# Optimization experiments

Hardware: AMD Instinct MI355X
Metric: run time of the kernel (lower is better)

Reference implementation:

```python
import jax, jax.numpy as jnp
import numpy as np

B, L, H, D = 1, 2048, 24, 128
BLKQ = BLKK = 64
TOPK_RATIO = 0.5


def setup_inputs() -> dict:
    key = jax.random.key(0)
    kq, kk, kv, kw = jax.random.split(key, 4)
    q = jax.random.normal(kq, (B, L, H, D), jnp.float32)
    k = jax.random.normal(kk, (B, L, H, D), jnp.float32)
    v = jax.random.normal(kv, (B, L, H, D), jnp.float32)
    proj_w = jax.random.normal(kw, (D, D), jnp.float32) * 0.02  # nn.Linear weight (out,in)
    proj_b = jnp.zeros((D,), jnp.float32)
    return {"query": q, "key": k, "value": v, "proj_w": proj_w, "proj_b": proj_b}


def _block_sparse_attention(q, k, v, scale):
    # q,k,v: (B,H,L,D). Block-mean pooled QK scores pick top-k key blocks per query block.
    Nq, Nk = L // BLKQ, L // BLKK
    topk = max(1, int(Nk * TOPK_RATIO))  # real_topk
    qb = q.reshape(B, H, Nq, BLKQ, D).mean(axis=3)          # (B,H,Nq,D)
    kb = k.reshape(B, H, Nk, BLKK, D).mean(axis=3)          # (B,H,Nk,D)
    blk_scores = jnp.einsum('bhqd,bhkd->bhqk', qb, kb)      # pooled block map
    _, lut = jax.lax.top_k(blk_scores, topk)                # (B,H,Nq,topk) selected key blocks
    kblk = k.reshape(B, H, Nk, BLKK, D)
    vblk = v.reshape(B, H, Nk, BLKK, D)
    idx = lut.reshape(B, H, Nq * topk, 1, 1)
    kg = jnp.take_along_axis(kblk, idx, axis=2).reshape(B, H, Nq, topk * BLKK, D)
    vg = jnp.take_along_axis(vblk, idx, axis=2).reshape(B, H, Nq, topk * BLKK, D)
    qr = q.reshape(B, H, Nq, BLKQ, D)
    scores = jnp.einsum('bhqid,bhqjd->bhqij', qr, kg) * scale  # (B,H,Nq,BLKQ,topk*BLKK)
    attn = jax.nn.softmax(scores, axis=-1)
    o = jnp.einsum('bhqij,bhqjd->bhqid', attn, vg)
    return o.reshape(B, H, L, D)


def _linear_attention(q, k, v):
    # feature_map='softmax' over the head dim
    ql = jax.nn.softmax(q, axis=-1)
    kl = jax.nn.softmax(k, axis=-1)
    kvsum = jnp.einsum('bhld,bhle->bhde', kl, v)            # K^T V  (B,H,D,D)
    ksum = kl.sum(axis=2)                                    # (B,H,D)
    num = jnp.einsum('bhld,bhde->bhle', ql, kvsum)
    den = 1e-5 + jnp.einsum('bhld,bhd->bhl', ql, ksum)[..., None]
    return num / den


def reference(query, key, value, proj_w, proj_b):
    q = jnp.swapaxes(query, 1, 2)  # (B,H,L,D)
    k = jnp.swapaxes(key, 1, 2)
    v = jnp.swapaxes(value, 1, 2)
    scale = D ** -0.5  # softmax_scale = head_size**-0.5
    o_s = _block_sparse_attention(q, k, v, scale)
    o_l = _linear_attention(q, k, v)
    o_l = o_l @ proj_w.T + proj_b  # learnable fusion projection
    out = jnp.swapaxes(o_s + o_l, 1, 2)  # back to (B,L,H,D)
    return out
```

## Files before the change

kernel.cpp:

```cpp
#include <hip/hip_runtime.h>
#include <math.h>

#define HH 24
#define LLEN 2048
#define DD 128
#define BLK 64
#define NBLK 32
#define TOPK 16
#define NCHUNK 16

typedef __attribute__((ext_vector_type(8))) short bf16x8;
typedef __attribute__((ext_vector_type(4))) float f32x4;

typedef unsigned int u32_g __attribute__((address_space(1)));
typedef unsigned int u32_l __attribute__((address_space(3)));

__device__ __forceinline__ unsigned short f2bf(float f) {
    unsigned u = __builtin_bit_cast(unsigned, f);
    unsigned r = (u + 0x7FFFu + ((u >> 16) & 1u)) >> 16;
    return (unsigned short)r;
}
__device__ __forceinline__ float bf2f(unsigned short b) {
    unsigned u = ((unsigned)b) << 16;
    return __builtin_bit_cast(float, u);
}
__device__ __forceinline__ void gload16(unsigned short* lds, const unsigned short* g) {
    __builtin_amdgcn_global_load_lds((const u32_g*)g, (u32_l*)lds, 16, 0, 0);
}

__global__ __launch_bounds__(256) void convert_pool(
    const float* __restrict__ q, const float* __restrict__ k, const float* __restrict__ v,
    unsigned short* __restrict__ kb16, unsigned short* __restrict__ vt16,
    float* __restrict__ qb, float* __restrict__ kb)
{
    const int nb = blockIdx.x, h = blockIdx.y;
    const int l0 = nb * BLK;
    const int tid = threadIdx.x;
    __shared__ unsigned short vt_s[DD * BLK];

    {
        const int r = tid >> 2, c0 = (tid & 3) * 4;
        const float* kp = k + ((size_t)(l0 + r) * HH + h) * DD + c0 * 8;
        unsigned short* krow = kb16 + ((size_t)h * LLEN + l0 + r) * DD;
        #pragma unroll
        for (int j = 0; j < 4; ++j) {
            float4 a = *(const float4*)(kp + j * 8);
            float4 c = *(const float4*)(kp + j * 8 + 4);
            unsigned short tmp[8] = {f2bf(a.x), f2bf(a.y), f2bf(a.z), f2bf(a.w),
                                     f2bf(c.x), f2bf(c.y), f2bf(c.z), f2bf(c.w)};
            const int chunk = (c0 + j) ^ (r & 7);
            *(bf16x8*)&krow[chunk * 8] = *(bf16x8*)tmp;
        }
    }
    {
        const int kp2 = tid >> 3, dgb = tid & 7;
        const float* v0p = v + ((size_t)(l0 + kp2 * 2) * HH + h) * DD;
        const float* v1p = v0p + (size_t)HH * DD;
        #pragma unroll
        for (int j2 = 0; j2 < 4; ++j2) {
            const int d0 = dgb * 4 + j2 * 32;
            float4 a = *(const float4*)(v0p + d0);
            float4 c = *(const float4*)(v1p + d0);
            float a4[4] = {a.x, a.y, a.z, a.w}, c4[4] = {c.x, c.y, c.z, c.w};
            #pragma unroll
            for (int i = 0; i < 4; ++i) {
                unsigned pak = (unsigned)f2bf(a4[i]) | ((unsigned)f2bf(c4[i]) << 16);
                const int d = d0 + i;
                const int chunk = (kp2 >> 2) ^ (d & 7);
                *(unsigned*)&vt_s[d * BLK + chunk * 8 + (kp2 & 3) * 2] = pak;
            }
        }
    }
    __syncthreads();
    {
        bf16x8* dstv = (bf16x8*)(vt16 + (size_t)(h * NBLK + nb) * DD * BLK);
        const bf16x8* srcv = (const bf16x8*)vt_s;
        #pragma unroll
        for (int j = 0; j < 4; ++j) dstv[tid * 4 + j] = srcv[tid * 4 + j];
    }
    __syncthreads();
    {
        float* ps = (float*)vt_s;
        const int d = tid & 127, half = tid >> 7;
        const size_t rs = (size_t)HH * DD;
        const float* qp = q + ((size_t)(l0 + half * 32) * HH + h) * DD + d;
        const float* kp = k + ((size_t)(l0 + half * 32) * HH + h) * DD + d;
        float sq = 0.f, sk = 0.f;
        #pragma unroll 8
        for (int i = 0; i < 32; ++i) { sq += qp[i * rs]; sk += kp[i * rs]; }
        ps[half * 128 + d] = sq;
        ps[256 + half * 128 + d] = sk;
        __syncthreads();
        if (half == 0) {
            qb[((size_t)h * NBLK + nb) * DD + d] = ps[d] + ps[128 + d];
            kb[((size_t)h * NBLK + nb) * DD + d] = ps[256 + d] + ps[384 + d];
        }
    }
}

__global__ __launch_bounds__(256) void topk_kernel(
    const float* __restrict__ qb, const float* __restrict__ kb, int* __restrict__ lut)
{
    const int h = blockIdx.x;
    __shared__ float kb_s[NBLK][DD];
    __shared__ float sc[NBLK][NBLK];
    const int tid = threadIdx.x;
    for (int f = tid; f < NBLK * DD / 4; f += 256)
        ((float4*)kb_s)[f] = ((const float4*)(kb + (size_t)h * NBLK * DD))[f];
    __syncthreads();
    for (int p = tid; p < NBLK * NBLK; p += 256) {
        const int iq = p >> 5, ik = p & 31;
        const float4* qr4 = (const float4*)(qb + ((size_t)h * NBLK + iq) * DD);
        const float4* kr4 = (const float4*)&kb_s[ik][0];
        float s = 0.f;
        for (int dq = 0; dq < DD / 4; ++dq) {
            float4 a = qr4[dq], b = kr4[dq];
            s += a.x * b.x + a.y * b.y + a.z * b.z + a.w * b.w;
        }
        sc[iq][ik] = s;
    }
    __syncthreads();
    if (tid < NBLK) {
        const int iq = tid;
        for (int t = 0; t < TOPK; ++t) {
            float bv = -1e30f; int bi = 0;
            for (int j = 0; j < NBLK; ++j) {
                float s = sc[iq][j];
                if (s > bv) { bv = s; bi = j; }
            }
            lut[((size_t)h * NBLK + iq) * TOPK + t] = bi;
            sc[iq][bi] = -1e30f;
        }
    }
}

__global__ __launch_bounds__(256, 2) void kv_mfma(
    const float* __restrict__ k, const unsigned short* __restrict__ vt16,
    float* __restrict__ kvp, float* __restrict__ ksp)
{
    const int h = blockIdx.x, c = blockIdx.y;
    __shared__ unsigned short klT[DD * DD];
    const int tid = threadIdx.x;
    const int quad = tid >> 3, dpart = tid & 7;
    const int d0 = dpart * 16;
    const int wid = tid >> 6, lane = tid & 63;
    const int l15 = lane & 15, g = lane >> 4;

    f32x4 acc[2][8];
    #pragma unroll
    for (int mi = 0; mi < 2; ++mi)
        #pragma unroll
        for (int nt = 0; nt < 8; ++nt) acc[mi][nt] = (f32x4){0.f, 0.f, 0.f, 0.f};
    float ksa[16];
    #pragma unroll
    for (int j = 0; j < 16; ++j) ksa[j] = 0.f;

    const int l0 = c * DD;
    {
        const int lr = quad * 4;
        float rows[4][16];
        #pragma unroll
        for (int i = 0; i < 4; ++i) {
            const float4* kp4 = (const float4*)(k + ((size_t)(l0 + lr + i) * HH + h) * DD + d0);
            #pragma unroll
            for (int t4 = 0; t4 < 4; ++t4) {
                float4 x = kp4[t4];
                rows[i][t4 * 4 + 0] = x.x; rows[i][t4 * 4 + 1] = x.y;
                rows[i][t4 * 4 + 2] = x.z; rows[i][t4 * 4 + 3] = x.w;
            }
        }
        #pragma unroll
        for (int i = 0; i < 4; ++i) {
            float mx = -1e30f;
            #pragma unroll
            for (int j = 0; j < 16; ++j) mx = fmaxf(mx, rows[i][j]);
            mx = fmaxf(mx, __shfl_xor(mx, 1));
            mx = fmaxf(mx, __shfl_xor(mx, 2));
            mx = fmaxf(mx, __shfl_xor(mx, 4));
            float s = 0.f;
            #pragma unroll
            for (int j = 0; j < 16; ++j) { rows[i][j] = __expf(rows[i][j] - mx); s += rows[i][j]; }
            s += __shfl_xor(s, 1);
            s += __shfl_xor(s, 2);
            s += __shfl_xor(s, 4);
            const float rinv = 1.0f / s;
            #pragma unroll
            for (int j = 0; j < 16; ++j) { rows[i][j] *= rinv; ksa[j] += rows[i][j]; }
        }
        #pragma unroll
        for (int j = 0; j < 16; ++j) {
            const int d = d0 + j;
            unsigned long long pk =
                (unsigned long long)f2bf(rows[0][j]) |
                ((unsigned long long)f2bf(rows[1][j]) << 16) |
                ((unsigned long long)f2bf(rows[2][j]) << 32) |
                ((unsigned long long)f2bf(rows[3][j]) << 48);
            const int chunk = (quad >> 1) ^ (d & 7);
            *(unsigned long long*)&klT[d * DD + chunk * 8 + (quad & 1) * 4] = pk;
        }
    }
    __syncthreads();
    const int bkt = c * 2;
    #pragma unroll
    for (int ks = 0; ks < 4; ++ks) {
        bf16x8 af[2];
        #pragma unroll
        for (int mi = 0; mi < 2; ++mi) {
            const int d = (wid * 2 + mi) * 16 + l15;
            const int chunk = (ks * 4 + g) ^ (d & 7);
            af[mi] = *(const bf16x8*)&klT[d * DD + chunk * 8];
        }
        const int s = ks * 4 + g;
        const int kt = bkt + (s >> 3);
        #pragma unroll
        for (int nt = 0; nt < 8; ++nt) {
            const int e = nt * 16 + l15;
            const int cc = (s & 7) ^ (e & 7);
            bf16x8 bf = *(const bf16x8*)&vt16[((size_t)(h * NBLK + kt) * DD + e) * BLK + cc * 8];
            acc[0][nt] = __builtin_amdgcn_mfma_f32_16x16x32_bf16(af[0], bf, acc[0][nt], 0, 0, 0);
            acc[1][nt] = __builtin_amdgcn_mfma_f32_16x16x32_bf16(af[1], bf, acc[1][nt], 0, 0, 0);
        }
    }
    float* op = kvp + ((size_t)h * NCHUNK + c) * DD * DD;
    #pragma unroll
    for (int mi = 0; mi < 2; ++mi)
        #pragma unroll
        for (int nt = 0; nt < 8; ++nt)
            #pragma unroll
            for (int r = 0; r < 4; ++r)
                op[(size_t)((wid * 2 + mi) * 16 + g * 4 + r) * DD + nt * 16 + l15] = acc[mi][nt][r];
    #pragma unroll
    for (int j = 0; j < 16; ++j) {
        ksa[j] += __shfl_xor(ksa[j], 8);
        ksa[j] += __shfl_xor(ksa[j], 16);
        ksa[j] += __shfl_xor(ksa[j], 32);
    }
    if ((lane >> 3) == 0) {
        float* kp2 = ksp + (((size_t)h * NCHUNK + c) * 4 + wid) * DD + d0;
        #pragma unroll
        for (int j = 0; j < 16; ++j) kp2[j] = ksa[j];
    }
}

__global__ __launch_bounds__(256) void reduce_M(
    const float* __restrict__ kvp, const float* __restrict__ ksp,
    const float* __restrict__ W, unsigned short* __restrict__ Mt,
    float* __restrict__ ksumf)
{
    const int h = blockIdx.x, rb = blockIdx.y;
    __shared__ float kv_s[32][DD];
    const int tid = threadIdx.x;
    for (int f4 = tid; f4 < 32 * DD / 4; f4 += 256) {
        float4 s = make_float4(0.f, 0.f, 0.f, 0.f);
        #pragma unroll
        for (int cc = 0; cc < NCHUNK; ++cc) {
            float4 x = ((const float4*)(kvp + ((size_t)h * NCHUNK + cc) * DD * DD
                                        + (size_t)rb * 32 * DD))[f4];
            s.x += x.x; s.y += x.y; s.z += x.z; s.w += x.w;
        }
        ((float4*)kv_s)[f4] = s;
    }
    if (rb == 0 && tid < DD) {
        float s = 0.f;
        #pragma unroll
        for (int p = 0; p < NCHUNK * 4; ++p)
            s += ksp[((size_t)h * NCHUNK * 4 + p) * DD + tid];
        ksumf[(size_t)h * DD + tid] = s;
    }
    __syncthreads();
    const int e = tid & 127, dh = tid >> 7;
    float accm[16];
    #pragma unroll
    for (int i = 0; i < 16; ++i) accm[i] = 0.f;
    const float4* wr4 = (const float4*)(W + (size_t)e * DD);
    for (int c4 = 0; c4 < DD / 4; ++c4) {
        const float4 wv = wr4[c4];
        #pragma unroll
        for (int i = 0; i < 16; ++i) {
            const float4 kv4 = ((const float4*)&kv_s[dh * 16 + i][0])[c4];
            accm[i] += kv4.x * wv.x + kv4.y * wv.y + kv4.z * wv.z + kv4.w * wv.w;
        }
    }
    unsigned short* mp = Mt + (size_t)h * DD * DD + (size_t)e * DD + rb * 32 + dh * 16;
    #pragma unroll
    for (int ii = 0; ii < 16; ii += 2) {
        unsigned pk = (unsigned)f2bf(accm[ii]) | ((unsigned)f2bf(accm[ii + 1]) << 16);
        *(unsigned*)&mp[ii] = pk;
    }
}

__global__ __launch_bounds__(256, 3) void sla_attn(
    const float* __restrict__ q, const unsigned short* __restrict__ kb16,
    const unsigned short* __restrict__ vt16, const int* __restrict__ lut,
    const unsigned short* __restrict__ Mt, const float* __restrict__ ksumf,
    const float* __restrict__ pb, float* __restrict__ out)
{
    const int b = blockIdx.x;
    const int slot = b >> 3;
    const int h = (b & 7) + 8 * (slot >> 5);
    const int nq = slot & 31;

    __shared__ unsigned short Ks[BLK * DD];
    __shared__ unsigned short Vt[DD * BLK];
    __shared__ unsigned short Ps[4 * 16 * BLK];

    const int tid = threadIdx.x;
    const int wid = tid >> 6, lane = tid & 63;
    const int l15 = lane & 15, g = lane >> 4;
    const int q0 = wid * 16;

    bf16x8 qf[4];
    {
        const float scale = 0.08838834764831845f;
        const int qrow = nq * BLK + q0 + l15;
        const float* qp = q + ((size_t)qrow * HH + h) * DD;
        #pragma unroll
        for (int ks = 0; ks < 4; ++ks) {
            const int d0 = ks * 32 + g * 8;
            float4 a = *(const float4*)(qp + d0);
            float4 c = *(const float4*)(qp + d0 + 4);
            float vv[8] = {a.x, a.y, a.z, a.w, c.x, c.y, c.z, c.w};
            #pragma unroll
            for (int j = 0; j < 8; ++j)
                qf[ks][j] = (short)f2bf(vv[j] * scale);
        }
    }

    f32x4 Oacc[8];
    #pragma unroll
    for (int nt = 0; nt < 8; ++nt) Oacc[nt] = (f32x4){0.f, 0.f, 0.f, 0.f};
    float m_run = -1e30f, l_run = 0.f;

    const int* lrow = lut + ((size_t)h * NBLK + nq) * TOPK;

    {
        const int kb0 = lrow[0];
        const unsigned short* kg = kb16 + ((size_t)h * LLEN + (size_t)kb0 * BLK) * DD;
        #pragma unroll
        for (int i = 0; i < 4; ++i) {
            const int is = wid * 4 + i;
            gload16(&Ks[is * 512], kg + is * 512 + lane * 8);
        }
    }

    for (int it = 0; it < TOPK; ++it) {
        const int kbI = lrow[it];
        __builtin_amdgcn_s_barrier();
        {
            const unsigned short* vg = vt16 + (size_t)(h * NBLK + kbI) * DD * BLK;
            #pragma unroll
            for (int i = 0; i < 4; ++i) {
                const int is = wid * 4 + i;
                gload16(&Vt[is * 512], vg + is * 512 + lane * 8);
            }
        }
        asm volatile("s_waitcnt vmcnt(4)" ::: "memory");
        __builtin_amdgcn_sched_barrier(0);

        f32x4 sacc[4];
        #pragma unroll
        for (int mt = 0; mt < 4; ++mt) sacc[mt] = (f32x4){0.f, 0.f, 0.f, 0.f};
        __builtin_amdgcn_s_setprio(1);
        #pragma unroll
        for (int ks = 0; ks < 4; ++ks) {
            #pragma unroll
            for (int mt = 0; mt < 4; ++mt) {
                const int row = mt * 16 + l15;
                const int chunk = (ks * 4 + g) ^ (row & 7);
                bf16x8 kf = *(const bf16x8*)&Ks[row * DD + chunk * 8];
                sacc[mt] = __builtin_amdgcn_mfma_f32_16x16x32_bf16(kf, qf[ks], sacc[mt], 0, 0, 0);
            }
        }
        __builtin_amdgcn_s_setprio(0);

        __builtin_amdgcn_s_barrier();
        if (it + 1 < TOPK) {
            const int kbN = lrow[it + 1];
            const unsigned short* kg = kb16 + ((size_t)h * LLEN + (size_t)kbN * BLK) * DD;
            #pragma unroll
            for (int i = 0; i < 4; ++i) {
                const int is = wid * 4 + i;
                gload16(&Ks[is * 512], kg + is * 512 + lane * 8);
            }
        }

        float sv[16];
        #pragma unroll
        for (int mt = 0; mt < 4; ++mt)
            #pragma unroll
            for (int r = 0; r < 4; ++r) sv[mt * 4 + r] = sacc[mt][r];
        float mx = -1e30f;
        #pragma unroll
        for (int i = 0; i < 16; ++i) mx = fmaxf(mx, sv[i]);
        mx = fmaxf(mx, __shfl_xor(mx, 16));
        mx = fmaxf(mx, __shfl_xor(mx, 32));
        const float mnew = fmaxf(m_run, mx);
        const float alpha = __expf(m_run - mnew);
        float ssum = 0.f;
        #pragma unroll
        for (int i = 0; i < 16; ++i) { sv[i] = __expf(sv[i] - mnew); ssum += sv[i]; }
        ssum += __shfl_xor(ssum, 16);
        ssum += __shfl_xor(ssum, 32);
        l_run = l_run * alpha + ssum;
        m_run = mnew;

        {
            unsigned short* pw = Ps + wid * (16 * BLK) + l15 * BLK;
            #pragma unroll
            for (int mt = 0; mt < 4; ++mt) {
                #pragma unroll
                for (int pr = 0; pr < 2; ++pr) {
                    const int key = mt * 16 + g * 4 + pr * 2;
                    unsigned pak = (unsigned)f2bf(sv[mt * 4 + pr * 2])
                                 | ((unsigned)f2bf(sv[mt * 4 + pr * 2 + 1]) << 16);
                    const int chunk = (key >> 3) ^ (l15 & 7);
                    *(unsigned*)&pw[chunk * 8 + (key & 7)] = pak;
                }
            }
        }

        if (it + 1 < TOPK) {
            asm volatile("s_waitcnt vmcnt(4)" ::: "memory");
        } else {
            asm volatile("s_waitcnt vmcnt(0)" ::: "memory");
        }
        __builtin_amdgcn_sched_barrier(0);

        {
            float ar[4];
            #pragma unroll
            for (int r = 0; r < 4; ++r) ar[r] = __shfl(alpha, g * 4 + r);
            #pragma unroll
            for (int nt = 0; nt < 8; ++nt) {
                Oacc[nt][0] *= ar[0]; Oacc[nt][1] *= ar[1];
                Oacc[nt][2] *= ar[2]; Oacc[nt][3] *= ar[3];
            }
            const unsigned short* prd = Ps + wid * (16 * BLK) + l15 * BLK;
            #pragma unroll
            for (int ks2 = 0; ks2 < 2; ++ks2) {
                const int pch = (g + 4 * ks2) ^ (l15 & 7);
                bf16x8 pa = *(const bf16x8*)&prd[pch * 8];
                __builtin_amdgcn_s_setprio(1);
                #pragma unroll
                for (int nt = 0; nt < 8; ++nt) {
                    const int drow = nt * 16 + l15;
                    const int vch = (g + 4 * ks2) ^ (drow & 7);
                    bf16x8 vf = *(const bf16x8*)&Vt[drow * BLK + vch * 8];
                    Oacc[nt] = __builtin_amdgcn_mfma_f32_16x16x32_bf16(pa, vf, Oacc[nt], 0, 0, 0);
                }
                __builtin_amdgcn_s_setprio(0);
            }
        }
    }

    float qv[32];
    {
        const float iscale = 11.313708498984761f;
        #pragma unroll
        for (int ks = 0; ks < 4; ++ks)
            #pragma unroll
            for (int j = 0; j < 8; ++j)
                qv[ks * 8 + j] = bf2f((unsigned short)qf[ks][j]) * iscale;
    }
    float mx2 = -1e30f;
    #pragma unroll
    for (int j = 0; j < 32; ++j) mx2 = fmaxf(mx2, qv[j]);
    mx2 = fmaxf(mx2, __shfl_xor(mx2, 16));
    mx2 = fmaxf(mx2, __shfl_xor(mx2, 32));
    float s2 = 0.f;
    #pragma unroll
    for (int j = 0; j < 32; ++j) { qv[j] = __expf(qv[j] - mx2); s2 += qv[j]; }
    s2 += __shfl_xor(s2, 16);
    s2 += __shfl_xor(s2, 32);
    const float rinv = 1.0f / s2;
    float den = 0.f;
    bf16x8 af[4];
    {
        const float* ksb = ksumf + (size_t)h * DD;
        #pragma unroll
        for (int ks = 0; ks < 4; ++ks) {
            const int dd0 = ks * 32 + g * 8;
            float4 k0 = *(const float4*)(ksb + dd0);
            float4 k1 = *(const float4*)(ksb + dd0 + 4);
            float kk[8] = {k0.x, k0.y, k0.z, k0.w, k1.x, k1.y, k1.z, k1.w};
            #pragma unroll
            for (int j = 0; j < 8; ++j) {
                const float ql = qv[ks * 8 + j] * rinv;
                af[ks][j] = (short)f2bf(ql);
                den += ql * kk[j];
            }
        }
    }
    den += __shfl_xor(den, 16);
    den += __shfl_xor(den, 32);
    const float dinv = 1.0f / (1e-5f + den);

    f32x4 acc2[8];
    #pragma unroll
    for (int nt = 0; nt < 8; ++nt) acc2[nt] = (f32x4){0.f, 0.f, 0.f, 0.f};
    {
        const unsigned short* mrow = Mt + (size_t)h * DD * DD;
        #pragma unroll
        for (int ks = 0; ks < 4; ++ks) {
            #pragma unroll
            for (int nt = 0; nt < 8; ++nt) {
                bf16x8 bf = *(const bf16x8*)&mrow[(size_t)(nt * 16 + l15) * DD + (ks * 4 + g) * 8];
                acc2[nt] = __builtin_amdgcn_mfma_f32_16x16x32_bf16(af[ks], bf, acc2[nt], 0, 0, 0);
            }
        }
    }

    float bias[8];
    #pragma unroll
    for (int nt = 0; nt < 8; ++nt) bias[nt] = pb[nt * 16 + l15];
    #pragma unroll
    for (int r = 0; r < 4; ++r) {
        const float linv = 1.0f / __shfl(l_run, g * 4 + r);
        const float di = __shfl(dinv, g * 4 + r);
        const int grow = nq * BLK + q0 + g * 4 + r;
        float* dst = out + ((size_t)grow * HH + h) * DD + l15;
        #pragma unroll
        for (int nt = 0; nt < 8; ++nt)
            dst[nt * 16] = Oacc[nt][r] * linv + acc2[nt][r] * di + bias[nt];
    }
}

extern "C" void kernel_launch(void* const* d_in, const int* in_sizes, int n_in,
                              void* d_out, int out_size, void* d_ws, size_t ws_size,
                              hipStream_t stream)
{
    (void)in_sizes; (void)n_in; (void)out_size; (void)ws_size;
    const float* q  = (const float*)d_in[0];
    const float* k  = (const float*)d_in[1];
    const float* v  = (const float*)d_in[2];
    const float* pw = (const float*)d_in[3];
    const float* pb = (const float*)d_in[4];
    float* out = (float*)d_out;
    char* ws = (char*)d_ws;
    size_t off = 0;
    int*   lut   = (int*)(ws + off);   off += (size_t)HH * NBLK * TOPK * 4;
    float* qb    = (float*)(ws + off); off += (size_t)HH * NBLK * DD * 4;
    float* kb    = (float*)(ws + off); off += (size_t)HH * NBLK * DD * 4;
    float* kvp   = (float*)(ws + off); off += (size_t)HH * NCHUNK * DD * DD * 4;
    float* ksp   = (float*)(ws + off); off += (size_t)HH * NCHUNK * 4 * DD * 4;
    unsigned short* Mt = (unsigned short*)(ws + off); off += (size_t)HH * DD * DD * 2;
    float* ksumf = (float*)(ws + off); off += (size_t)HH * DD * 4;
    unsigned short* kb16 = (unsigned short*)(ws + off); off += (size_t)HH * LLEN * DD * 2;
    unsigned short* vt16 = (unsigned short*)(ws + off); off += (size_t)HH * LLEN * DD * 2;

    convert_pool<<<dim3(NBLK, HH), 256, 0, stream>>>(q, k, v, kb16, vt16, qb, kb);
    topk_kernel<<<HH, 256, 0, stream>>>(qb, kb, lut);
    kv_mfma<<<dim3(HH, NCHUNK), 256, 0, stream>>>(k, vt16, kvp, ksp);
    reduce_M<<<dim3(HH, 4), 256, 0, stream>>>(kvp, ksp, pw, Mt, ksumf);
    sla_attn<<<NBLK * HH, 256, 0, stream>>>(q, kb16, vt16, lut, Mt, ksumf, pb, out);
}
```

Before: 138.9 us.

## Move key softmax feature map into convert_pool and restructure sla_attn load sync

convert_pool now also computes the softmax-over-D feature map of K, writes a transposed bf16 copy (klT16) and per-block K column sums. kv_mfma then reads that precomputed layout directly from global memory, with fewer chunks each covering more of L, and drops its LDS staging and ksum work. Separately, sla_attn replaces the partial vmcnt(4) waits and the prefetch of the next K block with full vmcnt(0) waits plus barriers, issuing the next K load after the P write. The changes cost an extra bf16 buffer write and read, and they reduce the overlap of loads with compute in the attention loop.

Result: slower. 146.3 us (+5.4%).

```diff
diff --git a/kernel.cpp b/kernel.cpp
--- a/kernel.cpp
+++ b/kernel.cpp
@@ -7,7 +7,7 @@
 #define BLK 64
 #define NBLK 32
 #define TOPK 16
-#define NCHUNK 16
+#define NCHUNK 8
 
 typedef __attribute__((ext_vector_type(8))) short bf16x8;
 typedef __attribute__((ext_vector_type(4))) float f32x4;
@@ -31,12 +31,14 @@
 __global__ __launch_bounds__(256) void convert_pool(
     const float* __restrict__ q, const float* __restrict__ k, const float* __restrict__ v,
     unsigned short* __restrict__ kb16, unsigned short* __restrict__ vt16,
+    unsigned short* __restrict__ klT16, float* __restrict__ ksump,
     float* __restrict__ qb, float* __restrict__ kb)
 {
     const int nb = blockIdx.x, h = blockIdx.y;
     const int l0 = nb * BLK;
     const int tid = threadIdx.x;
     __shared__ unsigned short vt_s[DD * BLK];
+    __shared__ float ks_s[4][DD];
 
     {
         const int r = tid >> 2, c0 = (tid & 3) * 4;
@@ -77,6 +79,80 @@
         const bf16x8* srcv = (const bf16x8*)vt_s;
         #pragma unroll
         for (int j = 0; j < 4; ++j) dstv[tid * 4 + j] = srcv[tid * 4 + j];
+    }
+    __syncthreads();
+    {
+        const int kp2 = tid >> 3, dgb = tid & 7;
+        const float* k0p = k + ((size_t)(l0 + kp2 * 2) * HH + h) * DD;
+        const float* k1p = k0p + (size_t)HH * DD;
+        float r0[16], r1[16];
+        #pragma unroll
+        for (int j2 = 0; j2 < 4; ++j2) {
+            const int d0 = dgb * 4 + j2 * 32;
+            float4 a = *(const float4*)(k0p + d0);
+            float4 c = *(const float4*)(k1p + d0);
+            r0[j2 * 4 + 0] = a.x; r0[j2 * 4 + 1] = a.y; r0[j2 * 4 + 2] = a.z; r0[j2 * 4 + 3] = a.w;
+            r1[j2 * 4 + 0] = c.x; r1[j2 * 4 + 1] = c.y; r1[j2 * 4 + 2] = c.z; r1[j2 * 4 + 3] = c.w;
+        }
+        float m0 = -1e30f, m1 = -1e30f;
+        #pragma unroll
+        for (int j = 0; j < 16; ++j) { m0 = fmaxf(m0, r0[j]); m1 = fmaxf(m1, r1[j]); }
+        m0 = fmaxf(m0, __shfl_xor(m0, 1)); m0 = fmaxf(m0, __shfl_xor(m0, 2)); m0 = fmaxf(m0, __shfl_xor(m0, 4));
+        m1 = fmaxf(m1, __shfl_xor(m1, 1)); m1 = fmaxf(m1, __shfl_xor(m1, 2)); m1 = fmaxf(m1, __shfl_xor(m1, 4));
+        float s0 = 0.f, s1 = 0.f;
+        #pragma unroll
+        for (int j = 0; j < 16; ++j) {
+            r0[j] = __expf(r0[j] - m0); s0 += r0[j];
+            r1[j] = __expf(r1[j] - m1); s1 += r1[j];
+        }
+        s0 += __shfl_xor(s0, 1); s0 += __shfl_xor(s0, 2); s0 += __shfl_xor(s0, 4);
+        s1 += __shfl_xor(s1, 1); s1 += __shfl_xor(s1, 2); s1 += __shfl_xor(s1, 4);
+        const float i0 = 1.0f / s0, i1 = 1.0f / s1;
+        float ksa[16];
+        #pragma unroll
+        for (int j = 0; j < 16; ++j) {
+            r0[j] *= i0; r1[j] *= i1;
+            ksa[j] = r0[j] + r1[j];
+        }
+        #pragma unroll
+        for (int j2 = 0; j2 < 4; ++j2) {
+            #pragma unroll
+            for (int i = 0; i < 4; ++i) {
+                const int j = j2 * 4 + i;
+                unsigned pak = (unsigned)f2bf(r0[j]) | ((unsigned)f2bf(r1[j]) << 16);
+                const int d = dgb * 4 + j2 * 32 + i;
+                const int chunk = (kp2 >> 2) ^ (d & 7);
+                *(unsigned*)&vt_s[d * BLK + chunk * 8 + (kp2 & 3) * 2] = pak;
+            }
+        }
+        #pragma unroll
+        for (int j = 0; j < 16; ++j) {
+            ksa[j] += __shfl_xor(ksa[j], 8);
+            ksa[j] += __shfl_xor(ksa[j], 16);
+            ksa[j] += __shfl_xor(ksa[j], 32);
+        }
+        if ((tid & 63) < 8) {
+            const int wid = tid >> 6;
+            #pragma unroll
+            for (int j2 = 0; j2 < 4; ++j2)
+                #pragma unroll
+                for (int i = 0; i < 4; ++i)
+                    ks_s[wid][dgb * 4 + j2 * 32 + i] = ksa[j2 * 4 + i];
+        }
+    }
+    __syncthreads();
+    {
+        bf16x8* dstk = (bf16x8*)(klT16 + (size_t)(h * NBLK + nb) * DD * BLK);
+        const bf16x8* srcv = (const bf16x8*)vt_s;
+        #pragma unroll
+        for (int j = 0; j < 4; ++j) {
+            const int u = tid * 4 + j;
+            const int e = u >> 3, c = u & 7;
+            dstk[u] = srcv[e * 8 + (c ^ (e & 7))];
+        }
+        if (tid < DD)
+            ksump[((size_t)h * NBLK + nb) * DD + tid] =
+                ks_s[0][tid] + ks_s[1][tid] + ks_s[2][tid] + ks_s[3][tid];
     }
     __syncthreads();
     {
@@ -135,14 +211,11 @@
 }
 
 __global__ __launch_bounds__(256, 2) void kv_mfma(
-    const float* __restrict__ k, const unsigned short* __restrict__ vt16,
-    float* __restrict__ kvp, float* __restrict__ ksp)
+    const unsigned short* __restrict__ klT16, const unsigned short* __restrict__ vt16,
+    float* __restrict__ kvp)
 {
     const int h = blockIdx.x, c = blockIdx.y;
-    __shared__ unsigned short klT[DD * DD];
     const int tid = threadIdx.x;
-    const int quad = tid >> 3, dpart = tid & 7;
-    const int d0 = dpart * 16;
     const int wid = tid >> 6, lane = tid & 63;
     const int l15 = lane & 15, g = lane >> 4;
 
@@ -151,72 +224,25 @@
     for (int mi = 0; mi < 2; ++mi)
         #pragma unroll
         for (int nt = 0; nt < 8; ++nt) acc[mi][nt] = (f32x4){0.f, 0.f, 0.f, 0.f};
-    float ksa[16];
-    #pragma unroll
-    for (int j = 0; j < 16; ++j) ksa[j] = 0.f;
-
-    const int l0 = c * DD;
-    {
-        const int lr = quad * 4;
-        float rows[4][16];
-        #pragma unroll
-        for (int i = 0; i < 4; ++i) {
-            const float4* kp4 = (const float4*)(k + ((size_t)(l0 + lr + i) * HH + h) * DD + d0);
-            #pragma unroll
-            for (int t4 = 0; t4 < 4; ++t4) {
-                float4 x = kp4[t4];
-                rows[i][t4 * 4 + 0] = x.x; rows[i][t4 * 4 + 1] = x.y;
-                rows[i][t4 * 4 + 2] = x.z; rows[i][t4 * 4 + 3] = x.w;
-            }
-        }
-        #pragma unroll
-        for (int i = 0; i < 4; ++i) {
-            float mx = -1e30f;
-            #pragma unroll
-            for (int j = 0; j < 16; ++j) mx = fmaxf(mx, rows[i][j]);
-            mx = fmaxf(mx, __shfl_xor(mx, 1));
-            mx = fmaxf(mx, __shfl_xor(mx, 2));
-            mx = fmaxf(mx, __shfl_xor(mx, 4));
-            float s = 0.f;
-            #pragma unroll
-            for (int j = 0; j < 16; ++j) { rows[i][j] = __expf(rows[i][j] - mx); s += rows[i][j]; }
-            s += __shfl_xor(s, 1);
-            s += __shfl_xor(s, 2);
-            s += __shfl_xor(s, 4);
-            const float rinv = 1.0f / s;
-            #pragma unroll
-            for (int j = 0; j < 16; ++j) { rows[i][j] *= rinv; ksa[j] += rows[i][j]; }
-        }
-        #pragma unroll
-        for (int j = 0; j < 16; ++j) {
-            const int d = d0 + j;
-            unsigned long long pk =
-                (unsigned long long)f2bf(rows[0][j]) |
-                ((unsigned long long)f2bf(rows[1][j]) << 16) |
-                ((unsigned long long)f2bf(rows[2][j]) << 32) |
-                ((unsigned long long)f2bf(rows[3][j]) << 48);
-            const int chunk = (quad >> 1) ^ (d & 7);
-            *(unsigned long long*)&klT[d * DD + chunk * 8 + (quad & 1) * 4] = pk;
-        }
-    }
-    __syncthreads();
-    const int bkt = c * 2;
-    #pragma unroll
-    for (int ks = 0; ks < 4; ++ks) {
+
+    #pragma unroll
+    for (int ks = 0; ks < 8; ++ks) {
+        const int s = ks * 32 + g * 8;
+        const int nb = c * 4 + (s >> 6);
+        const int off = s & 63;
+        const unsigned short* ab = klT16 + (size_t)(h * NBLK + nb) * DD * BLK;
+        const unsigned short* bb = vt16 + (size_t)(h * NBLK + nb) * DD * BLK;
         bf16x8 af[2];
         #pragma unroll
         for (int mi = 0; mi < 2; ++mi) {
             const int d = (wid * 2 + mi) * 16 + l15;
-            const int chunk = (ks * 4 + g) ^ (d & 7);
-            af[mi] = *(const bf16x8*)&klT[d * DD + chunk * 8];
-        }
-        const int s = ks * 4 + g;
-        const int kt = bkt + (s >> 3);
+            af[mi] = *(const bf16x8*)&ab[d * BLK + off];
+        }
         #pragma unroll
         for (int nt = 0; nt < 8; ++nt) {
             const int e = nt * 16 + l15;
-            const int cc = (s & 7) ^ (e & 7);
-            bf16x8 bf = *(const bf16x8*)&vt16[((size_t)(h * NBLK + kt) * DD + e) * BLK + cc * 8];
+            const int cc = (off >> 3) ^ (e & 7);
+            bf16x8 bf = *(const bf16x8*)&bb[e * BLK + cc * 8];
             acc[0][nt] = __builtin_amdgcn_mfma_f32_16x16x32_bf16(af[0], bf, acc[0][nt], 0, 0, 0);
             acc[1][nt] = __builtin_amdgcn_mfma_f32_16x16x32_bf16(af[1], bf, acc[1][nt], 0, 0, 0);
         }
@@ -229,21 +255,10 @@
             #pragma unroll
             for (int r = 0; r < 4; ++r)
                 op[(size_t)((wid * 2 + mi) * 16 + g * 4 + r) * DD + nt * 16 + l15] = acc[mi][nt][r];
-    #pragma unroll
-    for (int j = 0; j < 16; ++j) {
-        ksa[j] += __shfl_xor(ksa[j], 8);
-        ksa[j] += __shfl_xor(ksa[j], 16);
-        ksa[j] += __shfl_xor(ksa[j], 32);
-    }
-    if ((lane >> 3) == 0) {
-        float* kp2 = ksp + (((size_t)h * NCHUNK + c) * 4 + wid) * DD + d0;
-        #pragma unroll
-        for (int j = 0; j < 16; ++j) kp2[j] = ksa[j];
-    }
 }
 
 __global__ __launch_bounds__(256) void reduce_M(
-    const float* __restrict__ kvp, const float* __restrict__ ksp,
+    const float* __restrict__ kvp, const float* __restrict__ ksump,
     const float* __restrict__ W, unsigned short* __restrict__ Mt,
     float* __restrict__ ksumf)
 {
@@ -263,8 +278,8 @@
     if (rb == 0 && tid < DD) {
         float s = 0.f;
         #pragma unroll
-        for (int p = 0; p < NCHUNK * 4; ++p)
-            s += ksp[((size_t)h * NCHUNK * 4 + p) * DD + tid];
+        for (int p = 0; p < NBLK; ++p)
+            s += ksump[((size_t)h * NBLK + p) * DD + tid];
         ksumf[(size_t)h * DD + tid] = s;
     }
     __syncthreads();
@@ -345,7 +360,11 @@
 
     for (int it = 0; it < TOPK; ++it) {
         const int kbI = lrow[it];
+        asm volatile("s_waitcnt vmcnt(0)" ::: "memory");
+        __builtin_amdgcn_sched_barrier(0);
         __builtin_amdgcn_s_barrier();
+        __builtin_amdgcn_sched_barrier(0);
+
         {
             const unsigned short* vg = vt16 + (size_t)(h * NBLK + kbI) * DD * BLK;
             #pragma unroll
@@ -354,8 +373,6 @@
                 gload16(&Vt[is * 512], vg + is * 512 + lane * 8);
             }
         }
-        asm volatile("s_waitcnt vmcnt(4)" ::: "memory");
-        __builtin_amdgcn_sched_barrier(0);
 
         f32x4 sacc[4];
         #pragma unroll
@@ -372,17 +389,6 @@
             }
         }
         __builtin_amdgcn_s_setprio(0);
-
-        __builtin_amdgcn_s_barrier();
-        if (it + 1 < TOPK) {
-            const int kbN = lrow[it + 1];
-            const unsigned short* kg = kb16 + ((size_t)h * LLEN + (size_t)kbN * BLK) * DD;
-            #pragma unroll
-            for (int i = 0; i < 4; ++i) {
-                const int is = wid * 4 + i;
-                gload16(&Ks[is * 512], kg + is * 512 + lane * 8);
-            }
-        }
 
         float sv[16];
         #pragma unroll
@@ -419,12 +425,20 @@
             }
         }
 
+        asm volatile("s_waitcnt vmcnt(0)" ::: "memory");
+        __builtin_amdgcn_sched_barrier(0);
+        __builtin_amdgcn_s_barrier();
+        __builtin_amdgcn_sched_barrier(0);
+
         if (it + 1 < TOPK) {
-            asm volatile("s_waitcnt vmcnt(4)" ::: "memory");
-        } else {
-            asm volatile("s_waitcnt vmcnt(0)" ::: "memory");
-        }
-        __builtin_amdgcn_sched_barrier(0);
+            const int kbN = lrow[it + 1];
+            const unsigned short* kg = kb16 + ((size_t)h * LLEN + (size_t)kbN * BLK) * DD;
+            #pragma unroll
+            for (int i = 0; i < 4; ++i) {
+                const int is = wid * 4 + i;
+                gload16(&Ks[is * 512], kg + is * 512 + lane * 8);
+            }
+        }
 
         {
             float ar[4];
@@ -542,15 +556,16 @@
     float* qb    = (float*)(ws + off); off += (size_t)HH * NBLK * DD * 4;
     float* kb    = (float*)(ws + off); off += (size_t)HH * NBLK * DD * 4;
     float* kvp   = (float*)(ws + off); off += (size_t)HH * NCHUNK * DD * DD * 4;
-    float* ksp   = (float*)(ws + off); off += (size_t)HH * NCHUNK * 4 * DD * 4;
+    float* ksump = (float*)(ws + off); off += (size_t)HH * NBLK * DD * 4;
     unsigned short* Mt = (unsigned short*)(ws + off); off += (size_t)HH * DD * DD * 2;
     float* ksumf = (float*)(ws + off); off += (size_t)HH * DD * 4;
-    unsigned short* kb16 = (unsigned short*)(ws + off); off += (size_t)HH * LLEN * DD * 2;
-    unsigned short* vt16 = (unsigned short*)(ws + off); off += (size_t)HH * LLEN * DD * 2;
-
-    convert_pool<<<dim3(NBLK, HH), 256, 0, stream>>>(q, k, v, kb16, vt16, qb, kb);
+    unsigned short* kb16  = (unsigned short*)(ws + off); off += (size_t)HH * LLEN * DD * 2;
+    unsigned short* vt16  = (unsigned short*)(ws + off); off += (size_t)HH * LLEN * DD * 2;
+    unsigned short* klT16 = (unsigned short*)(ws + off); off += (size_t)HH * LLEN * DD * 2;
+
+    convert_pool<<<dim3(NBLK, HH), 256, 0, stream>>>(q, k, v, kb16, vt16, klT16, ksump, qb, kb);
     topk_kernel<<<HH, 256, 0, stream>>>(qb, kb, lut);
-    kv_mfma<<<dim3(HH, NCHUNK), 256, 0, stream>>>(k, vt16, kvp, ksp);
-    reduce_M<<<dim3(HH, 4), 256, 0, stream>>>(kvp, ksp, pw, Mt, ksumf);
+    kv_mfma<<<dim3(HH, NCHUNK), 256, 0, stream>>>(klT16, vt16, kvp);
+    reduce_M<<<dim3(HH, 4), 256, 0, stream>>>(kvp, ksump, pw, Mt, ksumf);
     sla_attn<<<NBLK * HH, 256, 0, stream>>>(q, kb16, vt16, lut, Mt, ksumf, pb, out);
 }
```
